# Performance work log

Hardware: AMD Instinct MI355X
Metric: run time of the kernel (lower is better)

The kernel has to match this reference:

```python
import jax, jax.numpy as jnp
import numpy as np
from jax import lax

KSIZE = 3
SIGMA = 0.8
BLOCK = 8
DCT_THRESH = 2.5
DCT_CLIP = 10.0
DWT_LAM = 0.05


def _gaussian_kernel(dtype):
    coords = jnp.arange(KSIZE, dtype=dtype) - (KSIZE - 1) / 2.0
    grid = coords[None, :] ** 2 + coords[:, None] ** 2
    k = jnp.exp(-grid / (2.0 * SIGMA * SIGMA))
    return k / k.sum()


def gaussian_blur(x):
    # depthwise 3x3 gaussian with reflect padding, groups=C
    C = x.shape[1]
    k = _gaussian_kernel(x.dtype)
    kernel = jnp.broadcast_to(k[None, None], (C, 1, KSIZE, KSIZE))
    pad = KSIZE // 2
    xp = jnp.pad(x, ((0, 0), (0, 0), (pad, pad), (pad, pad)), mode='reflect')
    return lax.conv_general_dilated(
        xp, kernel, window_strides=(1, 1), padding='VALID',
        dimension_numbers=('NCHW', 'OIHW', 'NCHW'), feature_group_count=C)


def block_dct_normalize(x):
    # 8x8 block "DCT" implemented (as in the source) via fft2().real, then
    # soft shrink of small coeffs + clip, then ifft2().real reconstruction.
    B, C, H, W = x.shape
    Ph, Pw = H // BLOCK, W // BLOCK  # H, W chosen as multiples of 8 -> no pad
    blocks = x.reshape(B, C, Ph, BLOCK, Pw, BLOCK).transpose(0, 1, 2, 4, 3, 5)
    coeff = jnp.fft.fft2(blocks, norm='ortho').real
    ca = jnp.abs(coeff)
    coeff = jnp.where(ca < DCT_THRESH, coeff * (ca / (DCT_THRESH + 1e-8)), coeff)
    coeff = jnp.clip(coeff, -DCT_CLIP, DCT_CLIP)
    rec = jnp.fft.ifft2(coeff.astype(jnp.complex64), norm='ortho').real
    rec = rec.transpose(0, 1, 2, 4, 3, 5).reshape(B, C, H, W)
    return rec.astype(x.dtype)


def haar_dwt2(x):
    # orthonormal 2x2 Haar analysis; sign/order conventions cancel in the
    # soft-threshold + inverse pipeline (soft_threshold is odd in sign)
    B, C, H, W = x.shape
    r = x.reshape(B, C, H // 2, 2, W // 2, 2)
    a, b = r[:, :, :, 0, :, 0], r[:, :, :, 0, :, 1]
    c, d = r[:, :, :, 1, :, 0], r[:, :, :, 1, :, 1]
    LL = (a + b + c + d) * 0.5
    LH = (a + b - c - d) * 0.5
    HL = (a - b + c - d) * 0.5
    HH = (a - b - c + d) * 0.5
    return LL, LH, HL, HH


def haar_idwt2(LL, LH, HL, HH):
    B, C, Hh, Wh = LL.shape
    a = (LL + LH + HL + HH) * 0.5
    b = (LL + LH - HL - HH) * 0.5
    c = (LL - LH + HL - HH) * 0.5
    d = (LL - LH - HL + HH) * 0.5
    top = jnp.stack([a, b], axis=-1)  # (B,C,Hh,Wh,2)
    bot = jnp.stack([c, d], axis=-1)
    r = jnp.stack([top, bot], axis=3)  # (B,C,Hh,2,Wh,2)
    return r.reshape(B, C, 2 * Hh, 2 * Wh)


def soft_threshold(x, lam):
    return jnp.sign(x) * jnp.maximum(jnp.abs(x) - lam, 0.0)


def wavelet_refine(x):
    LL, LH, HL, HH = haar_dwt2(x)
    return haar_idwt2(LL, soft_threshold(LH, DWT_LAM),
                      soft_threshold(HL, DWT_LAM),
                      soft_threshold(HH, DWT_LAM))


def setup_inputs() -> dict:
    key = jax.random.key(0)
    I = jax.random.uniform(key, (32, 3, 512, 512), dtype=jnp.float32)
    return {"I": I}


def reference(I):
    I_g = gaussian_blur(I)
    I_d = block_dct_normalize(I_g)
    R_d = I_g - I_d
    I_d_wave = wavelet_refine(I_d)
    R_d_wave = wavelet_refine(R_d)
    # input_mode='concat', residual_type='R_d'
    return jnp.concatenate([I_d_wave, R_d_wave], axis=1)
```

## Files before the change

kernel.cpp:

```cpp
#include <hip/hip_runtime.h>

#define HW 512
#define TW 64
#define TH 32
#define STR 68

__device__ constexpr float CT[8] = {0.3535533906f, 0.25f, 0.0f, -0.25f,
                                    -0.3535533906f, -0.25f, 0.0f, 0.25f};
__device__ constexpr float STt[8] = {0.0f, 0.25f, 0.3535533906f, 0.25f,
                                     0.0f, -0.25f, -0.3535533906f, -0.25f};

__device__ __forceinline__ int reflect512(int v) {
    v = v < 0 ? -v : v;
    v = v > 511 ? 1022 - v : v;
    return v;
}

__device__ __forceinline__ float softt(float x) {
    return copysignf(fmaxf(fabsf(x) - 0.05f, 0.0f), x);
}

__device__ __forceinline__ void haar_quad(float a, float b, float c, float d,
                                          float& oa, float& ob, float& oc, float& od) {
    float LL = (a + b + c + d) * 0.5f;
    float LH = (a + b - c - d) * 0.5f;
    float HL = (a - b + c - d) * 0.5f;
    float HH = (a - b - c + d) * 0.5f;
    LH = softt(LH); HL = softt(HL); HH = softt(HH);
    oa = (LL + LH + HL + HH) * 0.5f;
    ob = (LL + LH - HL - HH) * 0.5f;
    oc = (LL - LH + HL - HH) * 0.5f;
    od = (LL - LH - HL + HH) * 0.5f;
}

__launch_bounds__(256, 4)
__global__ void sas_fused(const float* __restrict__ in, float* __restrict__ out) {
    __shared__ float sIn[34 * STR];
    __shared__ float sBlur[TH * STR];
    __shared__ float sP[TH * STR];
    __shared__ float sQ[TH * STR];

    const int tid = threadIdx.x;
    const int p = blockIdx.y;
    const int tile = blockIdx.x;
    const int tx0 = (tile & 7) * TW;
    const int ty0 = (tile >> 3) * TH;
    const float* __restrict__ inP = in + (size_t)p * (HW * HW);

    for (int k = tid; k < 34 * 66; k += 256) {
        int r = k / 66;
        int c = k - r * 66;
        int gy = reflect512(ty0 + r - 1);
        int gx = reflect512(tx0 + c - 1);
        sIn[r * STR + c] = inP[gy * HW + gx];
    }
    __syncthreads();

    {
        const float e = 0.45783335f;
        const float inv_s = 1.0f / ((1.0f + 2.0f * e) * (1.0f + 2.0f * e));
        const int i = tid & 31;
        const int seg = tid >> 5;
        const float* r0 = &sIn[(i + 0) * STR + 8 * seg];
        const float* r1 = &sIn[(i + 1) * STR + 8 * seg];
        const float* r2 = &sIn[(i + 2) * STR + 8 * seg];
        float v[10];
#pragma unroll
        for (int k = 0; k < 10; ++k)
            v[k] = e * (r0[k] + r2[k]) + r1[k];
        float* w = &sBlur[i * STR + 8 * seg];
#pragma unroll
        for (int k = 0; k < 8; ++k)
            w[k] = (e * (v[k] + v[k + 2]) + v[k + 1]) * inv_s;
    }
    __syncthreads();

    float* const sT = sIn;

    auto rowpass = [&](const float* __restrict__ src) {
        const int m = tid & 31;
        const int bx = tid >> 5;
        const float* x = &src[m * STR + 8 * bx];
        float xv[8];
#pragma unroll
        for (int n = 0; n < 8; ++n) xv[n] = x[n];
        float* pd = &sP[m * STR + 8 * bx];
        float* qd = &sQ[m * STR + 8 * bx];
#pragma unroll
        for (int v = 0; v < 8; ++v) {
            float pp = 0.0f, qq = 0.0f;
#pragma unroll
            for (int n = 0; n < 8; ++n) {
                pp += xv[n] * CT[(n * v) & 7];
                qq += xv[n] * STt[(n * v) & 7];
            }
            pd[v] = pp;
            qd[v] = qq;
        }
    };

    auto colpass = [&](float* __restrict__ dst, bool nonlin) {
        const int v = tid & 63;
        const int g = tid >> 6;
        float pm[8], qm[8];
#pragma unroll
        for (int m = 0; m < 8; ++m) {
            pm[m] = sP[(8 * g + m) * STR + v];
            qm[m] = sQ[(8 * g + m) * STR + v];
        }
#pragma unroll
        for (int u = 0; u < 8; ++u) {
            float t = 0.0f;
#pragma unroll
            for (int m = 0; m < 8; ++m)
                t += pm[m] * CT[(u * m) & 7] - qm[m] * STt[(u * m) & 7];
            if (nonlin) {
                float ca = fabsf(t);
                t = (ca < 2.5f) ? t * (ca * 0.4f) : t;
                t = fminf(fmaxf(t, -10.0f), 10.0f);
            }
            dst[(8 * g + u) * STR + v] = t;
        }
    };

    rowpass(sBlur);            __syncthreads();
    colpass(sT, true);         __syncthreads();
    rowpass(sT);               __syncthreads();
    colpass(sT, false);        __syncthreads();

    {
        const int qx = tid & 15;
        const int qy = tid >> 4;
        const int y0 = 2 * qy, y1 = y0 + 1;
        const int x0 = 4 * qx;
        float4 d0 = *(const float4*)&sT[y0 * STR + x0];
        float4 d1 = *(const float4*)&sT[y1 * STR + x0];
        float4 g0 = *(const float4*)&sBlur[y0 * STR + x0];
        float4 g1 = *(const float4*)&sBlur[y1 * STR + x0];
        float4 r0 = make_float4(g0.x - d0.x, g0.y - d0.y, g0.z - d0.z, g0.w - d0.w);
        float4 r1 = make_float4(g1.x - d1.x, g1.y - d1.y, g1.z - d1.z, g1.w - d1.w);

        const int chId = (p / 3) * 6 + (p % 3);
        float* __restrict__ oI = out + ((size_t)chId << 18);
        float* __restrict__ oR = out + ((size_t)(chId + 3) << 18);
        const size_t base = (size_t)(ty0 + y0) * HW + (tx0 + x0);

        float4 w0, w1;
        haar_quad(d0.x, d0.y, d1.x, d1.y, w0.x, w0.y, w1.x, w1.y);
        haar_quad(d0.z, d0.w, d1.z, d1.w, w0.z, w0.w, w1.z, w1.w);
        *(float4*)&oI[base] = w0;
        *(float4*)&oI[base + HW] = w1;

        haar_quad(r0.x, r0.y, r1.x, r1.y, w0.x, w0.y, w1.x, w1.y);
        haar_quad(r0.z, r0.w, r1.z, r1.w, w0.z, w0.w, w1.z, w1.w);
        *(float4*)&oR[base] = w0;
        *(float4*)&oR[base + HW] = w1;
    }
}

extern "C" void kernel_launch(void* const* d_in, const int* in_sizes, int n_in,
                              void* d_out, int out_size, void* d_ws, size_t ws_size,
                              hipStream_t stream) {
    const float* I = (const float*)d_in[0];
    float* out = (float*)d_out;
    dim3 grid(128, 96);
    sas_fused<<<grid, dim3(256), 0, stream>>>(I, out);
}
```

Baseline: 332.9 us.

## Compute each 8x8 block per thread in registers with factored DFT butterflies

```diff
diff --git a/kernel.cpp b/kernel.cpp
--- a/kernel.cpp
+++ b/kernel.cpp
@@ -1,14 +1,6 @@
 #include <hip/hip_runtime.h>
 
 #define HW 512
-#define TW 64
-#define TH 32
-#define STR 68
-
-__device__ constexpr float CT[8] = {0.3535533906f, 0.25f, 0.0f, -0.25f,
-                                    -0.3535533906f, -0.25f, 0.0f, 0.25f};
-__device__ constexpr float STt[8] = {0.0f, 0.25f, 0.3535533906f, 0.25f,
-                                     0.0f, -0.25f, -0.3535533906f, -0.25f};
 
 __device__ __forceinline__ int reflect512(int v) {
     v = v < 0 ? -v : v;
@@ -33,128 +25,147 @@
     od = (LL - LH - HL + HH) * 0.5f;
 }
 
-__launch_bounds__(256, 4)
+#define RA 0.35355339059327373f
+#define RB 0.25f
+
+__device__ __forceinline__ void dft8_cos(const float* __restrict__ x, float* __restrict__ P) {
+    float e0 = x[0] + x[4], d0 = x[0] - x[4];
+    float e1 = x[2] + x[6];
+    float o0 = x[1] + x[5], m0 = x[1] - x[5];
+    float o1 = x[3] + x[7], m1 = x[3] - x[7];
+    float see = e0 + e1, dee = e0 - e1, soo = o0 + o1;
+    float dd = m0 - m1;
+    P[0] = RA * (see + soo);
+    P[4] = RA * (see - soo);
+    float p2 = RA * dee;
+    P[2] = p2; P[6] = p2;
+    float t0 = RA * d0, t1 = RB * dd;
+    P[1] = t0 + t1; P[7] = t0 + t1;
+    P[3] = t0 - t1; P[5] = t0 - t1;
+}
+
+__device__ __forceinline__ void dft8_sin(const float* __restrict__ x, float* __restrict__ Q) {
+    float d1 = x[2] - x[6];
+    float o0 = x[1] + x[5], m0 = x[1] - x[5];
+    float o1 = x[3] + x[7], m1 = x[3] - x[7];
+    float qq = m0 + m1;
+    Q[0] = 0.0f; Q[4] = 0.0f;
+    float q2 = RA * (o0 - o1);
+    Q[2] = q2; Q[6] = -q2;
+    float t0 = RB * qq, t1 = RA * d1;
+    Q[1] = t0 + t1; Q[7] = -(t0 + t1);
+    Q[3] = t0 - t1; Q[5] = -(t0 - t1);
+}
+
+__launch_bounds__(256, 2)
 __global__ void sas_fused(const float* __restrict__ in, float* __restrict__ out) {
-    __shared__ float sIn[34 * STR];
-    __shared__ float sBlur[TH * STR];
-    __shared__ float sP[TH * STR];
-    __shared__ float sQ[TH * STR];
+    const int lane = threadIdx.x & 63;
+    const int wv = threadIdx.x >> 6;
+    const int p = blockIdx.y;
+    const int by = blockIdx.x * 4 + wv;
+    const float* __restrict__ inP = in + (size_t)p * (HW * HW);
+    const int cx = lane * 8;
 
-    const int tid = threadIdx.x;
-    const int p = blockIdx.y;
-    const int tile = blockIdx.x;
-    const int tx0 = (tile & 7) * TW;
-    const int ty0 = (tile >> 3) * TH;
-    const float* __restrict__ inP = in + (size_t)p * (HW * HW);
+    float4 va[10], vb[10];
+#pragma unroll
+    for (int j = 0; j < 10; ++j) {
+        int gy = reflect512(by * 8 - 1 + j);
+        const float* r = inP + (size_t)gy * HW + cx;
+        va[j] = *(const float4*)r;
+        vb[j] = *(const float4*)(r + 4);
+    }
 
-    for (int k = tid; k < 34 * 66; k += 256) {
-        int r = k / 66;
-        int c = k - r * 66;
-        int gy = reflect512(ty0 + r - 1);
-        int gx = reflect512(tx0 + c - 1);
-        sIn[r * STR + c] = inP[gy * HW + gx];
+    float x[10][10];
+#pragma unroll
+    for (int j = 0; j < 10; ++j) {
+        float lft = __shfl_up(vb[j].w, 1);
+        float rgt = __shfl_down(va[j].x, 1);
+        if (lane == 0)  lft = va[j].y;
+        if (lane == 63) rgt = vb[j].z;
+        x[j][0] = lft;
+        x[j][1] = va[j].x; x[j][2] = va[j].y; x[j][3] = va[j].z; x[j][4] = va[j].w;
+        x[j][5] = vb[j].x; x[j][6] = vb[j].y; x[j][7] = vb[j].z; x[j][8] = vb[j].w;
+        x[j][9] = rgt;
     }
-    __syncthreads();
 
-    {
-        const float e = 0.45783335f;
-        const float inv_s = 1.0f / ((1.0f + 2.0f * e) * (1.0f + 2.0f * e));
-        const int i = tid & 31;
-        const int seg = tid >> 5;
-        const float* r0 = &sIn[(i + 0) * STR + 8 * seg];
-        const float* r1 = &sIn[(i + 1) * STR + 8 * seg];
-        const float* r2 = &sIn[(i + 2) * STR + 8 * seg];
+    const float e = 0.45783336f;
+    const float inv_s = 1.0f / ((1.0f + 2.0f * e) * (1.0f + 2.0f * e));
+    float B[8][8];
+#pragma unroll
+    for (int j = 0; j < 8; ++j) {
         float v[10];
 #pragma unroll
-        for (int k = 0; k < 10; ++k)
-            v[k] = e * (r0[k] + r2[k]) + r1[k];
-        float* w = &sBlur[i * STR + 8 * seg];
+        for (int c = 0; c < 10; ++c)
+            v[c] = e * (x[j][c] + x[j + 2][c]) + x[j + 1][c];
 #pragma unroll
-        for (int k = 0; k < 8; ++k)
-            w[k] = (e * (v[k] + v[k + 2]) + v[k + 1]) * inv_s;
+        for (int c = 0; c < 8; ++c)
+            B[j][c] = (e * (v[c] + v[c + 2]) + v[c + 1]) * inv_s;
     }
-    __syncthreads();
 
-    float* const sT = sIn;
-
-    auto rowpass = [&](const float* __restrict__ src) {
-        const int m = tid & 31;
-        const int bx = tid >> 5;
-        const float* x = &src[m * STR + 8 * bx];
-        float xv[8];
+    float P[8][8], Q[8][8];
 #pragma unroll
-        for (int n = 0; n < 8; ++n) xv[n] = x[n];
-        float* pd = &sP[m * STR + 8 * bx];
-        float* qd = &sQ[m * STR + 8 * bx];
+    for (int m = 0; m < 8; ++m) { dft8_cos(B[m], P[m]); dft8_sin(B[m], Q[m]); }
 #pragma unroll
-        for (int v = 0; v < 8; ++v) {
-            float pp = 0.0f, qq = 0.0f;
+    for (int v = 0; v < 8; ++v) {
+        float pc[8], qc[8], tc[8], sc[8];
 #pragma unroll
-            for (int n = 0; n < 8; ++n) {
-                pp += xv[n] * CT[(n * v) & 7];
-                qq += xv[n] * STt[(n * v) & 7];
-            }
-            pd[v] = pp;
-            qd[v] = qq;
-        }
-    };
-
-    auto colpass = [&](float* __restrict__ dst, bool nonlin) {
-        const int v = tid & 63;
-        const int g = tid >> 6;
-        float pm[8], qm[8];
-#pragma unroll
-        for (int m = 0; m < 8; ++m) {
-            pm[m] = sP[(8 * g + m) * STR + v];
-            qm[m] = sQ[(8 * g + m) * STR + v];
-        }
+        for (int m = 0; m < 8; ++m) { pc[m] = P[m][v]; qc[m] = Q[m][v]; }
+        dft8_cos(pc, tc);
+        dft8_sin(qc, sc);
 #pragma unroll
         for (int u = 0; u < 8; ++u) {
-            float t = 0.0f;
+            float t = tc[u] - sc[u];
+            float ca = fabsf(t);
+            t = (ca < 2.5f) ? t * (ca * 0.4f) : t;
+            t = fminf(fmaxf(t, -10.0f), 10.0f);
+            P[u][v] = t;
+        }
+    }
 #pragma unroll
-            for (int m = 0; m < 8; ++m)
-                t += pm[m] * CT[(u * m) & 7] - qm[m] * STt[(u * m) & 7];
-            if (nonlin) {
-                float ca = fabsf(t);
-                t = (ca < 2.5f) ? t * (ca * 0.4f) : t;
-                t = fminf(fmaxf(t, -10.0f), 10.0f);
-            }
-            dst[(8 * g + u) * STR + v] = t;
+    for (int m = 0; m < 8; ++m) {
+        float tr[8];
+#pragma unroll
+        for (int n = 0; n < 8; ++n) tr[n] = P[m][n];
+        dft8_cos(tr, P[m]);
+        dft8_sin(tr, Q[m]);
+    }
+#pragma unroll
+    for (int v = 0; v < 8; ++v) {
+        float pc[8], qc[8], tc[8], sc[8];
+#pragma unroll
+        for (int m = 0; m < 8; ++m) { pc[m] = P[m][v]; qc[m] = Q[m][v]; }
+        dft8_cos(pc, tc);
+        dft8_sin(qc, sc);
+#pragma unroll
+        for (int u = 0; u < 8; ++u) P[u][v] = tc[u] - sc[u];
+    }
+
+    const int chId = (p / 3) * 6 + (p % 3);
+    float* __restrict__ oI = out + ((size_t)chId << 18);
+    float* __restrict__ oR = out + ((size_t)(chId + 3) << 18);
+#pragma unroll
+    for (int qy = 0; qy < 4; ++qy) {
+        float ti[2][8], tr_[2][8];
+#pragma unroll
+        for (int qx = 0; qx < 4; ++qx) {
+            float d00 = P[2*qy][2*qx],   d01 = P[2*qy][2*qx+1];
+            float d10 = P[2*qy+1][2*qx], d11 = P[2*qy+1][2*qx+1];
+            haar_quad(d00, d01, d10, d11,
+                      ti[0][2*qx], ti[0][2*qx+1], ti[1][2*qx], ti[1][2*qx+1]);
+            float r00 = B[2*qy][2*qx]   - d00, r01 = B[2*qy][2*qx+1]   - d01;
+            float r10 = B[2*qy+1][2*qx] - d10, r11 = B[2*qy+1][2*qx+1] - d11;
+            haar_quad(r00, r01, r10, r11,
+                      tr_[0][2*qx], tr_[0][2*qx+1], tr_[1][2*qx], tr_[1][2*qx+1]);
         }
-    };
-
-    rowpass(sBlur);            __syncthreads();
-    colpass(sT, true);         __syncthreads();
-    rowpass(sT);               __syncthreads();
-    colpass(sT, false);        __syncthreads();
-
-    {
-        const int qx = tid & 15;
-        const int qy = tid >> 4;
-        const int y0 = 2 * qy, y1 = y0 + 1;
-        const int x0 = 4 * qx;
-        float4 d0 = *(const float4*)&sT[y0 * STR + x0];
-        float4 d1 = *(const float4*)&sT[y1 * STR + x0];
-        float4 g0 = *(const float4*)&sBlur[y0 * STR + x0];
-        float4 g1 = *(const float4*)&sBlur[y1 * STR + x0];
-        float4 r0 = make_float4(g0.x - d0.x, g0.y - d0.y, g0.z - d0.z, g0.w - d0.w);
-        float4 r1 = make_float4(g1.x - d1.x, g1.y - d1.y, g1.z - d1.z, g1.w - d1.w);
-
-        const int chId = (p / 3) * 6 + (p % 3);
-        float* __restrict__ oI = out + ((size_t)chId << 18);
-        float* __restrict__ oR = out + ((size_t)(chId + 3) << 18);
-        const size_t base = (size_t)(ty0 + y0) * HW + (tx0 + x0);
-
-        float4 w0, w1;
-        haar_quad(d0.x, d0.y, d1.x, d1.y, w0.x, w0.y, w1.x, w1.y);
-        haar_quad(d0.z, d0.w, d1.z, d1.w, w0.z, w0.w, w1.z, w1.w);
-        *(float4*)&oI[base] = w0;
-        *(float4*)&oI[base + HW] = w1;
-
-        haar_quad(r0.x, r0.y, r1.x, r1.y, w0.x, w0.y, w1.x, w1.y);
-        haar_quad(r0.z, r0.w, r1.z, r1.w, w0.z, w0.w, w1.z, w1.w);
-        *(float4*)&oR[base] = w0;
-        *(float4*)&oR[base + HW] = w1;
+        size_t base = (size_t)(by * 8 + 2 * qy) * HW + cx;
+        *(float4*)&oI[base]          = make_float4(ti[0][0], ti[0][1], ti[0][2], ti[0][3]);
+        *(float4*)&oI[base + 4]      = make_float4(ti[0][4], ti[0][5], ti[0][6], ti[0][7]);
+        *(float4*)&oI[base + HW]     = make_float4(ti[1][0], ti[1][1], ti[1][2], ti[1][3]);
+        *(float4*)&oI[base + HW + 4] = make_float4(ti[1][4], ti[1][5], ti[1][6], ti[1][7]);
+        *(float4*)&oR[base]          = make_float4(tr_[0][0], tr_[0][1], tr_[0][2], tr_[0][3]);
+        *(float4*)&oR[base + 4]      = make_float4(tr_[0][4], tr_[0][5], tr_[0][6], tr_[0][7]);
+        *(float4*)&oR[base + HW]     = make_float4(tr_[1][0], tr_[1][1], tr_[1][2], tr_[1][3]);
+        *(float4*)&oR[base + HW + 4] = make_float4(tr_[1][4], tr_[1][5], tr_[1][6], tr_[1][7]);
     }
 }
 
@@ -163,6 +174,6 @@
                               hipStream_t stream) {
     const float* I = (const float*)d_in[0];
     float* out = (float*)d_out;
-    dim3 grid(128, 96);
+    dim3 grid(16, 96);
     sas_fused<<<grid, dim3(256), 0, stream>>>(I, out);
 }
```

Measured after the change: 279.3 us. 1.19x faster.
